# Kernel tuning notes

Measured on AMD Instinct MI355X. Metric: run time of the kernel, lower is better.

Reference implementation:

```python
import jax, jax.numpy as jnp
import numpy as np
import math

N_EMBD = 1024
N_HEAD = 16
HEAD_SIZE = N_EMBD // N_HEAD
LAYER_IDX = 2
LAMBDA_INIT = 0.8 - 0.6 * math.exp(-0.3 * (LAYER_IDX - 1))
LN_EPS = 1e-5
B, T = 4, 1024


def setup_inputs() -> dict:
    key = jax.random.key(0)
    ks = jax.random.split(key, 11)
    s = 0.02  # weight init scale
    return {
        "x": jax.random.normal(ks[0], (B, T, N_EMBD), dtype=jnp.float32),
        "Wq1": jax.random.normal(ks[1], (N_EMBD, N_EMBD), dtype=jnp.float32) * s,
        "Wq2": jax.random.normal(ks[2], (N_EMBD, N_EMBD), dtype=jnp.float32) * s,
        "Wk1": jax.random.normal(ks[3], (N_EMBD, N_EMBD), dtype=jnp.float32) * s,
        "Wk2": jax.random.normal(ks[4], (N_EMBD, N_EMBD), dtype=jnp.float32) * s,
        "Wv": jax.random.normal(ks[5], (N_EMBD, 2 * N_EMBD), dtype=jnp.float32) * s,
        "Wc": jax.random.normal(ks[6], (2 * N_EMBD, N_EMBD), dtype=jnp.float32) * s,
        "lq1": jax.random.normal(ks[7], (N_HEAD, HEAD_SIZE), dtype=jnp.float32) * 0.1,
        "lk1": jax.random.normal(ks[8], (N_HEAD, HEAD_SIZE), dtype=jnp.float32) * 0.1,
        "lq2": jax.random.normal(ks[9], (N_HEAD, HEAD_SIZE), dtype=jnp.float32) * 0.1,
        "lk2": jax.random.normal(ks[10], (N_HEAD, HEAD_SIZE), dtype=jnp.float32) * 0.1,
    }


def reference(x, Wq1, Wq2, Wk1, Wk2, Wv, Wc, lq1, lk1, lq2, lk2):
    Bx, Tx, C = x.shape
    H, hs = N_HEAD, HEAD_SIZE
    scale = 1.0 / math.sqrt(hs)

    # projections -> (B, T, H, d)
    q1 = (x @ Wq1).reshape(Bx, Tx, H, hs)
    q2 = (x @ Wq2).reshape(Bx, Tx, H, hs)
    k1 = (x @ Wk1).reshape(Bx, Tx, H, hs)
    k2 = (x @ Wk2).reshape(Bx, Tx, H, hs)
    v = (x @ Wv).reshape(Bx, Tx, H, 2 * hs)

    # dual score streams (B, H, T, T)
    att1 = jnp.einsum("bqhd,bkhd->bhqk", q1, k1) * scale
    att2 = jnp.einsum("bqhd,bkhd->bhqk", q2, k2) * scale

    causal = jnp.tril(jnp.ones((Tx, Tx), dtype=bool))  # (T, T)
    neg_inf = jnp.float32(-jnp.inf)
    att1 = jnp.where(causal, att1, neg_inf)
    att2 = jnp.where(causal, att2, neg_inf)
    a1 = jax.nn.softmax(att1, axis=-1)
    a2 = jax.nn.softmax(att2, axis=-1)

    # per-head differential lambda
    lam1 = jnp.exp(jnp.sum(lq1 * lk1, axis=-1))  # (H,)
    lam2 = jnp.exp(jnp.sum(lq2 * lk2, axis=-1))  # (H,)
    lam_full = lam1 - lam2 + LAMBDA_INIT  # (H,)

    att = a1 - lam_full[None, :, None, None] * a2  # dropout = identity (eval)

    # PV matmul -> (B, T, H, 2*hs)
    y = jnp.einsum("bhqk,bkhd->bqhd", att, v)

    # subLN over last dim (no affine)
    mu = jnp.mean(y, axis=-1, keepdims=True)
    var = jnp.mean(jnp.square(y - mu), axis=-1, keepdims=True)
    y = (y - mu) / jnp.sqrt(var + LN_EPS)
    y = y * (1.0 - LAMBDA_INIT)

    y = y.reshape(Bx, Tx, 2 * C)
    return y @ Wc  # resid dropout = identity (eval)
```

## Files before the change

kernel.cpp:

```cpp
#include <hip/hip_runtime.h>


#define T_SEQ 1024
#define NH 16
#define DV 128
#define NPROJ 6144
#define KSTR 72

typedef __bf16 bf16_t;
typedef __bf16 bf16x8 __attribute__((ext_vector_type(8)));
typedef __bf16 bf16x4 __attribute__((ext_vector_type(4)));
typedef __bf16 bf16x2 __attribute__((ext_vector_type(2)));
typedef _Float16 f16x4 __attribute__((ext_vector_type(4)));
typedef _Float16 f16x2 __attribute__((ext_vector_type(2)));
typedef short s16x4 __attribute__((ext_vector_type(4)));
typedef float f32x4 __attribute__((ext_vector_type(4)));

#define LAMBDA_INIT 0.35550906759096928f
#define ONE_MINUS_LI 0.6444909324090307f
#define LOG2E 1.4426950408889634f
#define RTHR 44.36f

#if __has_builtin(__builtin_amdgcn_mfma_f32_16x16x16_bf16)
#define MFMA16(a, b, c) __builtin_amdgcn_mfma_f32_16x16x16_bf16(a, b, c, 0, 0, 0)
#elif __has_builtin(__builtin_amdgcn_mfma_f32_16x16x16bf16_1k)
#define MFMA16(a, b, c)                                                       \
  __builtin_amdgcn_mfma_f32_16x16x16bf16_1k(                                  \
      __builtin_bit_cast(s16x4, a), __builtin_bit_cast(s16x4, b), c, 0, 0, 0)
#else
#define MFMA16(a, b, c) (c)
#endif

#define MFMA32(a, b, c) __builtin_amdgcn_mfma_f32_16x16x32_bf16(a, b, c, 0, 0, 0)

#define GLDS(g, l)                                                            \
  __builtin_amdgcn_global_load_lds(                                           \
      (const __attribute__((address_space(1))) void*)(g),                     \
      (__attribute__((address_space(3))) void*)(l), 16, 0, 0)

static const size_t OFF_WCAT = 0;
static const size_t OFF_XB = OFF_WCAT + (size_t)6144 * 1024 * 2;
static const size_t OFF_WCT = OFF_XB + (size_t)4096 * 1024 * 2;
static const size_t OFF_PROJ = OFF_WCT + (size_t)2048 * 1024 * 2;
static const size_t OFF_VT = OFF_PROJ + (size_t)4096 * 6144 * 2;
static const size_t OFF_YLN = OFF_VT + (size_t)64 * 128 * 1024 * 2;
static const size_t OFF_LAM = OFF_YLN + (size_t)4096 * 2048 * 2;

__global__ void __launch_bounds__(256) cast_x(const float* __restrict__ x,
                                              bf16_t* __restrict__ o) {
  const int i = (blockIdx.x * 256 + threadIdx.x) * 4;
  float4 v = *(const float4*)(x + i);
  bf16x4 r = {(bf16_t)v.x, (bf16_t)v.y, (bf16_t)v.z, (bf16_t)v.w};
  *(bf16x4*)(o + i) = r;
}

__device__ __forceinline__ void tcast_body(const float* __restrict__ W,
                                           bf16_t* __restrict__ Wt, int K,
                                           int N, int row0) {
  __shared__ float tile[32][33];
  const int k0 = blockIdx.x * 32, n0 = blockIdx.y * 32;
  const int tx = threadIdx.x & 31, ty = threadIdx.x >> 5;
#pragma unroll
  for (int i = 0; i < 32; i += 8)
    tile[ty + i][tx] = W[(long)(k0 + ty + i) * N + n0 + tx];
  __syncthreads();
#pragma unroll
  for (int i = 0; i < 32; i += 8)
    Wt[(long)(row0 + n0 + ty + i) * K + k0 + tx] = (bf16_t)tile[tx][ty + i];
}

__global__ void __launch_bounds__(256) tcast_w(const float* __restrict__ W,
                                               bf16_t* __restrict__ Wt, int K,
                                               int N, int row0) {
  tcast_body(W, Wt, K, N, row0);
}

__global__ void __launch_bounds__(256) tcast_w4(const float* __restrict__ W0,
                                                const float* __restrict__ W1,
                                                const float* __restrict__ W2,
                                                const float* __restrict__ W3,
                                                bf16_t* __restrict__ Wt) {
  const float* Ws[4] = {W0, W1, W2, W3};
  tcast_body(Ws[blockIdx.z], Wt, 1024, 1024, blockIdx.z * 1024);
}

__global__ void lam_kernel(const float* __restrict__ lq1,
                           const float* __restrict__ lk1,
                           const float* __restrict__ lq2,
                           const float* __restrict__ lk2,
                           float* __restrict__ lam) {
  const int h = threadIdx.x;
  if (h < NH) {
    float d1 = 0.f, d2 = 0.f;
    for (int i = 0; i < 64; ++i) {
      d1 += lq1[h * 64 + i] * lk1[h * 64 + i];
      d2 += lq2[h * 64 + i] * lk2[h * 64 + i];
    }
    lam[h] = expf(d1) - expf(d2) + LAMBDA_INIT;
  }
}

#define GBM 256
#define GBN 256
#define GBK 64

__global__ void __launch_bounds__(512, 1) gemm256(const bf16_t* __restrict__ A,
                                                  const bf16_t* __restrict__ Bt,
                                                  bf16_t* __restrict__ C,
                                                  int M, int N, int K,
                                                  int nbx) {
  __shared__ __align__(16) bf16_t As[2][GBM * GBK];
  __shared__ __align__(16) bf16_t Bs[2][GBN * GBK];
  const int tid = threadIdx.x;
  const int w = tid >> 6, lane = tid & 63;
  const int quad = lane >> 4, l16 = lane & 15;
  const int wr = w >> 2, wc = w & 3;

  const int wg = blockIdx.x;
  const int cpx = gridDim.x >> 3;
  const int sw = (wg & 7) * cpx + (wg >> 3);
  const int by = sw / nbx, bx = sw % nbx;
  const int m0 = by * GBM, n0 = bx * GBN;

  const int r8 = lane >> 3, g = lane & 7;
  const int gsw = (g ^ r8) * 8;
  const bf16_t* gA[4];
  const bf16_t* gB[4];
#pragma unroll
  for (int j = 0; j < 4; ++j) {
    gA[j] = A + (long)(m0 + w * 32 + j * 8 + r8) * K + gsw;
    gB[j] = Bt + (long)(n0 + w * 32 + j * 8 + r8) * K + gsw;
  }

  const int kx = (l16 & 7) << 4;
  const int ko0 = (quad * 16) ^ kx;
  const int ko1 = (64 + quad * 16) ^ kx;

  f32x4 acc[8][4] = {};

  const int nt = K >> 6;

#pragma unroll
  for (int j = 0; j < 4; ++j) {
    GLDS(gA[j], As[0] + (w * 32 + j * 8) * GBK);
    GLDS(gB[j], Bs[0] + (w * 32 + j * 8) * GBK);
  }
  asm volatile("s_waitcnt vmcnt(0)" ::: "memory");
  __builtin_amdgcn_s_barrier();

  for (int t = 0; t < nt; ++t) {
    const bf16_t* Ab = (t & 1) ? As[1] : As[0];
    const bf16_t* Bb = (t & 1) ? Bs[1] : Bs[0];
    bf16_t* Asb = (t & 1) ? As[0] : As[1];
    bf16_t* Bsb = (t & 1) ? Bs[0] : Bs[1];
    const bool pf = (t + 1 < nt);
    const long ko = (long)(t + 1) * GBK;

    const char* Arow = (const char*)Ab + (size_t)(wr * 128 + l16) * 128;
    const char* Brow = (const char*)Bb + (size_t)(wc * 64 + l16) * 128;

    bf16x8 af[4][2], bn0[2][2], bn1[2][2];

#pragma unroll
    for (int mt = 0; mt < 4; ++mt) {
      af[mt][0] = *(const bf16x8*)(Arow + (size_t)mt * 16 * 128 + ko0);
      af[mt][1] = *(const bf16x8*)(Arow + (size_t)mt * 16 * 128 + ko1);
    }
#pragma unroll
    for (int n = 0; n < 2; ++n) {
      bn0[n][0] = *(const bf16x8*)(Brow + (size_t)n * 16 * 128 + ko0);
      bn0[n][1] = *(const bf16x8*)(Brow + (size_t)n * 16 * 128 + ko1);
    }
    if (pf) {
      GLDS(gA[0] + ko, Asb + (w * 32) * GBK);
      GLDS(gB[0] + ko, Bsb + (w * 32) * GBK);
      GLDS(gA[1] + ko, Asb + (w * 32 + 8) * GBK);
      GLDS(gB[1] + ko, Bsb + (w * 32 + 8) * GBK);
    }
    __builtin_amdgcn_s_barrier();
    __builtin_amdgcn_s_setprio(1);
#pragma unroll
    for (int mt = 0; mt < 4; ++mt)
#pragma unroll
      for (int n = 0; n < 2; ++n) {
        acc[mt][n] = MFMA32(af[mt][0], bn0[n][0], acc[mt][n]);
        acc[mt][n] = MFMA32(af[mt][1], bn0[n][1], acc[mt][n]);
      }
    __builtin_amdgcn_s_setprio(0);
    __builtin_amdgcn_s_barrier();

#pragma unroll
    for (int n = 0; n < 2; ++n) {
      bn1[n][0] = *(const bf16x8*)(Brow + (size_t)(32 + n * 16) * 128 + ko0);
      bn1[n][1] = *(const bf16x8*)(Brow + (size_t)(32 + n * 16) * 128 + ko1);
    }
    if (pf) {
      GLDS(gA[2] + ko, Asb + (w * 32 + 16) * GBK);
      GLDS(gB[2] + ko, Bsb + (w * 32 + 16) * GBK);
      GLDS(gA[3] + ko, Asb + (w * 32 + 24) * GBK);
      GLDS(gB[3] + ko, Bsb + (w * 32 + 24) * GBK);
    }
    __builtin_amdgcn_s_barrier();
    __builtin_amdgcn_s_setprio(1);
#pragma unroll
    for (int mt = 0; mt < 4; ++mt)
#pragma unroll
      for (int n = 0; n < 2; ++n) {
        acc[mt][2 + n] = MFMA32(af[mt][0], bn1[n][0], acc[mt][2 + n]);
        acc[mt][2 + n] = MFMA32(af[mt][1], bn1[n][1], acc[mt][2 + n]);
      }
    __builtin_amdgcn_s_setprio(0);
    __builtin_amdgcn_s_barrier();

#pragma unroll
    for (int mt = 0; mt < 4; ++mt) {
      af[mt][0] = *(const bf16x8*)(Arow + (size_t)(64 + mt * 16) * 128 + ko0);
      af[mt][1] = *(const bf16x8*)(Arow + (size_t)(64 + mt * 16) * 128 + ko1);
    }
    __builtin_amdgcn_s_barrier();
    __builtin_amdgcn_s_setprio(1);
#pragma unroll
    for (int mt = 0; mt < 4; ++mt)
#pragma unroll
      for (int n = 0; n < 2; ++n) {
        acc[4 + mt][2 + n] = MFMA32(af[mt][0], bn1[n][0], acc[4 + mt][2 + n]);
        acc[4 + mt][2 + n] = MFMA32(af[mt][1], bn1[n][1], acc[4 + mt][2 + n]);
      }
    __builtin_amdgcn_s_setprio(0);
    __builtin_amdgcn_s_barrier();

    __builtin_amdgcn_s_setprio(1);
#pragma unroll
    for (int mt = 0; mt < 4; ++mt)
#pragma unroll
      for (int n = 0; n < 2; ++n) {
        acc[4 + mt][n] = MFMA32(af[mt][0], bn0[n][0], acc[4 + mt][n]);
        acc[4 + mt][n] = MFMA32(af[mt][1], bn0[n][1], acc[4 + mt][n]);
      }
    __builtin_amdgcn_s_setprio(0);

    asm volatile("s_waitcnt vmcnt(0)" ::: "memory");
    __builtin_amdgcn_s_barrier();
  }

#pragma unroll
  for (int mt = 0; mt < 8; ++mt)
#pragma unroll
    for (int n = 0; n < 4; ++n) {
      const int col = n0 + wc * 64 + n * 16 + l16;
#pragma unroll
      for (int i = 0; i < 4; ++i) {
        const int row = m0 + wr * 128 + mt * 16 + quad * 4 + i;
        C[(long)row * N + col] = (bf16_t)acc[mt][n][i];
      }
    }
}

#define BM 128
#define BK 32

template <typename OutT>
__global__ void __launch_bounds__(256) gemm_bt_n64(const bf16_t* __restrict__ A,
                                                   const bf16_t* __restrict__ Bt,
                                                   OutT* __restrict__ C, int M,
                                                   int N, int K) {
  __shared__ __align__(16) bf16_t As[BM * BK];
  __shared__ __align__(16) bf16_t Bs[64 * BK];
  const int tid = threadIdx.x;
  const int w = tid >> 6;
  const int lane = tid & 63;
  const int quad = lane >> 4, l16 = lane & 15;
  const int m0 = blockIdx.y * BM, n0 = blockIdx.x * 64;
  const int wm = (w >> 1) * 64, wn = (w & 1) * 32;
  const int srow = tid >> 2;
  const int scol = (tid & 3) * 8;

  const bf16_t* Ag0 = A + (long)(m0 + srow) * K + scol;
  const bf16_t* Ag1 = Ag0 + (long)64 * K;
  const bf16_t* Bg0 = Bt + (long)(n0 + srow) * K + scol;
  bf16_t* lA0 = As + tid * 8;
  bf16_t* lA1 = As + 2048 + tid * 8;
  bf16_t* lB0 = Bs + tid * 8;

  f32x4 acc[4][2] = {};

  for (int k0 = 0; k0 < K; k0 += BK) {
    GLDS(Ag0 + k0, lA0);
    GLDS(Ag1 + k0, lA1);
    GLDS(Bg0 + k0, lB0);
    __syncthreads();
    bf16x8 af[4], bfr[2];
#pragma unroll
    for (int t = 0; t < 4; ++t)
      af[t] = *(const bf16x8*)(As + (wm + t * 16 + l16) * BK + quad * 8);
#pragma unroll
    for (int t = 0; t < 2; ++t)
      bfr[t] = *(const bf16x8*)(Bs + (wn + t * 16 + l16) * BK + quad * 8);
#pragma unroll
    for (int mt = 0; mt < 4; ++mt)
#pragma unroll
      for (int ntt = 0; ntt < 2; ++ntt)
        acc[mt][ntt] = MFMA32(af[mt], bfr[ntt], acc[mt][ntt]);
    __syncthreads();
  }

#pragma unroll
  for (int mt = 0; mt < 4; ++mt)
#pragma unroll
    for (int ntt = 0; ntt < 2; ++ntt) {
      const int col = n0 + wn + ntt * 16 + l16;
#pragma unroll
      for (int i = 0; i < 4; ++i) {
        const int row = m0 + wm + mt * 16 + quad * 4 + i;
        C[(long)row * N + col] = (OutT)acc[mt][ntt][i];
      }
    }
}

__global__ void __launch_bounds__(256) transpose_v(const bf16_t* __restrict__ proj,
                                                   bf16_t* __restrict__ vt) {
  __shared__ bf16_t tile[32][34];
  const int bh = blockIdx.z;
  const int b = bh >> 4, h = bh & 15;
  const int t0 = blockIdx.x * 32, d0 = blockIdx.y * 32;
  const int tx = threadIdx.x & 31, ty = threadIdx.x >> 5;
  const bf16_t* src = proj + (long)(b * T_SEQ) * NPROJ + 4096 + h * 128;
#pragma unroll
  for (int i = 0; i < 32; i += 8)
    tile[ty + i][tx] = src[(long)(t0 + ty + i) * NPROJ + d0 + tx];
  __syncthreads();
  bf16_t* dst = vt + ((long)bh * DV) * T_SEQ;
#pragma unroll
  for (int i = 0; i < 32; i += 8)
    dst[(long)(d0 + ty + i) * T_SEQ + t0 + tx] = tile[tx][ty + i];
}

__global__ void __launch_bounds__(256) attn_kernel(const bf16_t* __restrict__ proj,
                                                   const bf16_t* __restrict__ vt,
                                                   _Float16* __restrict__ a1,
                                                   _Float16* __restrict__ a2) {
  const int x = blockIdx.x;
  const int qblk = 15 - (x >> 7);
  const int st = (x >> 6) & 1;
  const int bh = x & 63;
  const int b = bh >> 4, h = bh & 15;
  const int tid = threadIdx.x;
  const int w = tid >> 6, lane = tid & 63;
  const int quad = lane >> 4, l16 = lane & 15;
  const long bT = (long)b * T_SEQ;

  __shared__ __align__(16) bf16_t Ks[64 * KSTR];
  __shared__ __align__(16) bf16_t Vs[DV * KSTR];

  const int koff = h * 64 + 2048 + st * 1024;
  const bf16_t* gK = proj + (bT + (tid >> 2)) * (long)NPROJ + koff + (tid & 3) * 16;
  const bf16_t* gV = vt + (long)bh * DV * T_SEQ + (long)(tid >> 1) * T_SEQ +
                     (tid & 1) * 32;
  const int kwK = (tid >> 2) * KSTR + (tid & 3) * 16;
  const int kwV = (tid >> 1) * KSTR + (tid & 1) * 32;

  const float sc = 0.125f * LOG2E;
  const int q0 = qblk * 64 + w * 16;
  const int qg = q0 + l16;

  const bf16_t* qrow = proj + (bT + qg) * (long)NPROJ + h * 64 + st * 1024;
  bf16x8 aq[2];
  aq[0] = *(const bf16x8*)(qrow + quad * 8);
  aq[1] = *(const bf16x8*)(qrow + 32 + quad * 8);

  f32x4 O[8] = {};
  float m = -3.0e38f, l = 0.f;
  const bf16x4 one4 = {(bf16_t)1.0f, (bf16_t)1.0f, (bf16_t)1.0f, (bf16_t)1.0f};

  const int kend_blk = qblk * 64 + 64;
  const int kend_w = q0 + 16;

  bf16x8 rK[2], rV[4];
  rK[0] = *(const bf16x8*)(gK);
  rK[1] = *(const bf16x8*)(gK + 8);
#pragma unroll
  for (int j = 0; j < 4; ++j) rV[j] = *(const bf16x8*)(gV + j * 8);

  for (int kt = 0; kt < kend_blk; kt += 64) {
    *(bf16x8*)(Ks + kwK) = rK[0];
    *(bf16x8*)(Ks + kwK + 8) = rK[1];
#pragma unroll
    for (int j = 0; j < 4; ++j) *(bf16x8*)(Vs + kwV + j * 8) = rV[j];
    __syncthreads();

    if (kt + 64 < kend_blk) {
      const long ko = (long)(kt + 64) * NPROJ;
      rK[0] = *(const bf16x8*)(gK + ko);
      rK[1] = *(const bf16x8*)(gK + ko + 8);
#pragma unroll
      for (int j = 0; j < 4; ++j)
        rV[j] = *(const bf16x8*)(gV + kt + 64 + j * 8);
    }

    if (kt < kend_w) {
      f32x4 s[4];
#pragma unroll
      for (int c = 0; c < 4; ++c) {
        const bf16_t* kr = Ks + (c * 16 + l16) * KSTR;
        bf16x8 ka0 = *(const bf16x8*)(kr + quad * 8);
        bf16x8 ka1 = *(const bf16x8*)(kr + 32 + quad * 8);
        f32x4 z = {};
        z = MFMA32(ka0, aq[0], z);
        z = MFMA32(ka1, aq[1], z);
        s[c] = z;
      }
      if (kt + 63 > q0) {
#pragma unroll
        for (int c = 0; c < 4; ++c)
#pragma unroll
          for (int i = 0; i < 4; ++i) {
            const int key = kt + c * 16 + quad * 4 + i;
            if (key > qg) s[c][i] = -1e30f;
          }
      }
      float t[4];
#pragma unroll
      for (int c = 0; c < 4; ++c)
        t[c] = fmaxf(fmaxf(s[c][0], s[c][1]), fmaxf(s[c][2], s[c][3]));
      float mx = fmaxf(fmaxf(t[0], t[1]), fmaxf(t[2], t[3]));
      mx = fmaxf(mx, __shfl_xor(mx, 16));
      mx = fmaxf(mx, __shfl_xor(mx, 32));
      if (!__all(mx <= m + RTHR)) {
        const float mn = fmaxf(m, mx);
        const float al = exp2f((m - mn) * sc);
        m = mn;
#pragma unroll
        for (int f = 0; f < 8; ++f)
#pragma unroll
          for (int i = 0; i < 4; ++i) O[f][i] *= al;
        l *= al;
      }
      const float ms = m * sc;
      bf16x4 pc[4];
#pragma unroll
      for (int c = 0; c < 4; ++c)
#pragma unroll
        for (int i = 0; i < 4; ++i)
          pc[c][i] = (bf16_t)exp2f(fmaf(s[c][i], sc, -ms));
      f32x4 la = {};
#pragma unroll
      for (int c = 0; c < 4; ++c) la = MFMA16(one4, pc[c], la);
#pragma unroll
      for (int c = 0; c < 4; ++c) {
#pragma unroll
        for (int f = 0; f < 8; ++f) {
          bf16x4 va =
              *(const bf16x4*)(Vs + (f * 16 + l16) * KSTR + c * 16 + quad * 4);
          O[f] = MFMA16(va, pc[c], O[f]);
        }
      }
      l += la[0];
    }
    __syncthreads();
  }

  const float inv = 1.0f / l;
  _Float16* ob = st ? a2 : a1;
  _Float16* dst = ob + ((bT + qg) * 16 + h) * (long)128 + quad * 4;
#pragma unroll
  for (int f = 0; f < 8; ++f) {
    f16x4 o = {(_Float16)(O[f][0] * inv), (_Float16)(O[f][1] * inv),
               (_Float16)(O[f][2] * inv), (_Float16)(O[f][3] * inv)};
    *(f16x4*)(dst + f * 16) = o;
  }
}

__global__ void __launch_bounds__(256) combine_kernel(const _Float16* __restrict__ a1,
                                                      const _Float16* __restrict__ a2,
                                                      const float* __restrict__ lamp,
                                                      bf16_t* __restrict__ yln) {
  const int unit = blockIdx.x * 4 + (threadIdx.x >> 6);
  const int lane = threadIdx.x & 63;
  const float lam = lamp[unit & 15];
  const long base = (long)unit * 128 + lane * 2;
  f16x2 v1 = *(const f16x2*)(a1 + base);
  f16x2 v2 = *(const f16x2*)(a2 + base);
  float y0 = (float)v1[0] - lam * (float)v2[0];
  float y1 = (float)v1[1] - lam * (float)v2[1];
  float sm = y0 + y1, sq = y0 * y0 + y1 * y1;
#pragma unroll
  for (int off = 1; off < 64; off <<= 1) {
    sm += __shfl_xor(sm, off);
    sq += __shfl_xor(sq, off);
  }
  const float mu = sm * (1.0f / 128.0f);
  const float var = sq * (1.0f / 128.0f) - mu * mu;
  const float rs = rsqrtf(var + 1e-5f) * ONE_MINUS_LI;
  bf16x2 o = {(bf16_t)((y0 - mu) * rs), (bf16_t)((y1 - mu) * rs)};
  *(bf16x2*)(yln + base) = o;
}

extern "C" void kernel_launch(void* const* d_in, const int* in_sizes, int n_in,
                              void* d_out, int out_size, void* d_ws,
                              size_t ws_size, hipStream_t stream) {
  const float* x = (const float*)d_in[0];
  const float* Wq1 = (const float*)d_in[1];
  const float* Wq2 = (const float*)d_in[2];
  const float* Wk1 = (const float*)d_in[3];
  const float* Wk2 = (const float*)d_in[4];
  const float* Wv = (const float*)d_in[5];
  const float* Wc = (const float*)d_in[6];
  const float* lq1 = (const float*)d_in[7];
  const float* lk1 = (const float*)d_in[8];
  const float* lq2 = (const float*)d_in[9];
  const float* lk2 = (const float*)d_in[10];
  float* out = (float*)d_out;

  char* ws = (char*)d_ws;
  bf16_t* wcat = (bf16_t*)(ws + OFF_WCAT);
  bf16_t* xb = (bf16_t*)(ws + OFF_XB);
  bf16_t* wct = (bf16_t*)(ws + OFF_WCT);
  bf16_t* projb = (bf16_t*)(ws + OFF_PROJ);
  bf16_t* vtb = (bf16_t*)(ws + OFF_VT);
  bf16_t* ylnb = (bf16_t*)(ws + OFF_YLN);
  float* lamp = (float*)(ws + OFF_LAM);
  _Float16* a1b = (_Float16*)(ws + OFF_YLN);
  _Float16* a2b = (_Float16*)(ws + OFF_WCAT);

  cast_x<<<4096, 256, 0, stream>>>(x, xb);
  tcast_w4<<<dim3(32, 32, 4), 256, 0, stream>>>(Wq1, Wq2, Wk1, Wk2, wcat);
  tcast_w<<<dim3(32, 64), 256, 0, stream>>>(Wv, wcat, 1024, 2048, 4096);
  tcast_w<<<dim3(64, 32), 256, 0, stream>>>(Wc, wct, 2048, 1024, 0);
  lam_kernel<<<1, 64, 0, stream>>>(lq1, lk1, lq2, lk2, lamp);

  gemm256<<<dim3(384), 512, 0, stream>>>(xb, wcat, projb, 4096, 6144, 1024, 24);
  transpose_v<<<dim3(32, 4, 64), 256, 0, stream>>>(projb, vtb);
  attn_kernel<<<dim3(2048), 256, 0, stream>>>(projb, vtb, a1b, a2b);
  combine_kernel<<<dim3(16384), 256, 0, stream>>>(a1b, a2b, lamp, ylnb);
  gemm_bt_n64<float><<<dim3(16, 32), 256, 0, stream>>>(ylnb, wct, out, 4096, 1024, 2048);
}
```

Measured before the change: 304.5 us.

## Pair causal q-blocks per attention block, permute V layout, widen output GEMM tile

Each attention workgroup now processes two complementary query blocks (15-p and p) sequentially, so the causal triangle's work is balanced per block and half as many blocks are launched. The V transpose writes keys in a permuted order so the PV loop can fetch 8 bf16 per LDS read and split them across two 16x16x16 MFMAs. The final projection GEMM uses 128x128 tiles instead of 128x64, raising per-wave reuse. In exchange there are fewer blocks for latency hiding and more accumulator registers in the GEMM.

```diff
diff --git a/kernel.cpp b/kernel.cpp
--- a/kernel.cpp
+++ b/kernel.cpp
@@ -257,62 +257,65 @@
 }
 
 #define BM 128
+#define BN 128
 #define BK 32
 
 template <typename OutT>
-__global__ void __launch_bounds__(256) gemm_bt_n64(const bf16_t* __restrict__ A,
-                                                   const bf16_t* __restrict__ Bt,
-                                                   OutT* __restrict__ C, int M,
-                                                   int N, int K) {
+__global__ void __launch_bounds__(256) gemm_bt(const bf16_t* __restrict__ A,
+                                               const bf16_t* __restrict__ Bt,
+                                               OutT* __restrict__ C, int M,
+                                               int N, int K) {
   __shared__ __align__(16) bf16_t As[BM * BK];
-  __shared__ __align__(16) bf16_t Bs[64 * BK];
+  __shared__ __align__(16) bf16_t Bs[BN * BK];
   const int tid = threadIdx.x;
   const int w = tid >> 6;
   const int lane = tid & 63;
   const int quad = lane >> 4, l16 = lane & 15;
-  const int m0 = blockIdx.y * BM, n0 = blockIdx.x * 64;
-  const int wm = (w >> 1) * 64, wn = (w & 1) * 32;
+  const int m0 = blockIdx.y * BM, n0 = blockIdx.x * BN;
+  const int wm = (w >> 1) * 64, wn = (w & 1) * 64;
   const int srow = tid >> 2;
   const int scol = (tid & 3) * 8;
 
   const bf16_t* Ag0 = A + (long)(m0 + srow) * K + scol;
   const bf16_t* Ag1 = Ag0 + (long)64 * K;
   const bf16_t* Bg0 = Bt + (long)(n0 + srow) * K + scol;
+  const bf16_t* Bg1 = Bg0 + (long)64 * K;
   bf16_t* lA0 = As + tid * 8;
   bf16_t* lA1 = As + 2048 + tid * 8;
   bf16_t* lB0 = Bs + tid * 8;
-
-  f32x4 acc[4][2] = {};
+  bf16_t* lB1 = Bs + 2048 + tid * 8;
+
+  f32x4 acc[4][4] = {};
 
   for (int k0 = 0; k0 < K; k0 += BK) {
     GLDS(Ag0 + k0, lA0);
     GLDS(Ag1 + k0, lA1);
     GLDS(Bg0 + k0, lB0);
+    GLDS(Bg1 + k0, lB1);
     __syncthreads();
-    bf16x8 af[4], bfr[2];
-#pragma unroll
-    for (int t = 0; t < 4; ++t)
+    bf16x8 af[4], bfr[4];
+#pragma unroll
+    for (int t = 0; t < 4; ++t) {
       af[t] = *(const bf16x8*)(As + (wm + t * 16 + l16) * BK + quad * 8);
-#pragma unroll
-    for (int t = 0; t < 2; ++t)
       bfr[t] = *(const bf16x8*)(Bs + (wn + t * 16 + l16) * BK + quad * 8);
+    }
 #pragma unroll
     for (int mt = 0; mt < 4; ++mt)
 #pragma unroll
-      for (int ntt = 0; ntt < 2; ++ntt)
-        acc[mt][ntt] = MFMA32(af[mt], bfr[ntt], acc[mt][ntt]);
+      for (int nt = 0; nt < 4; ++nt)
+        acc[mt][nt] = MFMA32(af[mt], bfr[nt], acc[mt][nt]);
     __syncthreads();
   }
 
 #pragma unroll
   for (int mt = 0; mt < 4; ++mt)
 #pragma unroll
-    for (int ntt = 0; ntt < 2; ++ntt) {
-      const int col = n0 + wn + ntt * 16 + l16;
+    for (int nt = 0; nt < 4; ++nt) {
+      const int col = n0 + wn + nt * 16 + l16;
 #pragma unroll
       for (int i = 0; i < 4; ++i) {
         const int row = m0 + wm + mt * 16 + quad * 4 + i;
-        C[(long)row * N + col] = (OutT)acc[mt][ntt][i];
+        C[(long)row * N + col] = (OutT)acc[mt][nt][i];
       }
     }
 }
@@ -329,10 +332,14 @@
   for (int i = 0; i < 32; i += 8)
     tile[ty + i][tx] = src[(long)(t0 + ty + i) * NPROJ + d0 + tx];
   __syncthreads();
-  bf16_t* dst = vt + ((long)bh * DV) * T_SEQ;
-#pragma unroll
-  for (int i = 0; i < 32; i += 8)
-    dst[(long)(d0 + ty + i) * T_SEQ + t0 + tx] = tile[tx][ty + i];
+  const int d_loc = threadIdx.x >> 3;
+  const int g = threadIdx.x & 7;
+  const int s = g >> 2, qd = g & 3;
+  const int tl = s * 16 + qd * 4;
+  bf16x4 o = {tile[tl + 0][d_loc], tile[tl + 1][d_loc], tile[tl + 2][d_loc],
+              tile[tl + 3][d_loc]};
+  bf16_t* dst = vt + (long)bh * (DV * T_SEQ) + (long)(d0 + d_loc) * T_SEQ;
+  *(bf16x4*)(dst + t0 + qd * 8 + s * 4) = o;
 }
 
 __global__ void __launch_bounds__(256) attn_kernel(const bf16_t* __restrict__ proj,
@@ -340,7 +347,7 @@
                                                    _Float16* __restrict__ a1,
                                                    _Float16* __restrict__ a2) {
   const int x = blockIdx.x;
-  const int qblk = 15 - (x >> 7);
+  const int p = x >> 7;
   const int st = (x >> 6) & 1;
   const int bh = x & 63;
   const int b = bh >> 4, h = bh & 15;
@@ -354,119 +361,128 @@
 
   const int koff = h * 64 + 2048 + st * 1024;
   const bf16_t* gK = proj + (bT + (tid >> 2)) * (long)NPROJ + koff + (tid & 3) * 16;
-  const bf16_t* gV = vt + (long)bh * DV * T_SEQ + (long)(tid >> 1) * T_SEQ +
-                     (tid & 1) * 32;
+  const bf16_t* gV = vt + (long)bh * DV * T_SEQ + (long)(tid >> 3) * T_SEQ +
+                     (tid & 7) * 8;
   const int kwK = (tid >> 2) * KSTR + (tid & 3) * 16;
-  const int kwV = (tid >> 1) * KSTR + (tid & 1) * 32;
+  const int kwV = (tid >> 3) * KSTR + (tid & 7) * 8;
 
   const float sc = 0.125f * LOG2E;
-  const int q0 = qblk * 64 + w * 16;
-  const int qg = q0 + l16;
-
-  const bf16_t* qrow = proj + (bT + qg) * (long)NPROJ + h * 64 + st * 1024;
-  bf16x8 aq[2];
-  aq[0] = *(const bf16x8*)(qrow + quad * 8);
-  aq[1] = *(const bf16x8*)(qrow + 32 + quad * 8);
-
-  f32x4 O[8] = {};
-  float m = -3.0e38f, l = 0.f;
   const bf16x4 one4 = {(bf16_t)1.0f, (bf16_t)1.0f, (bf16_t)1.0f, (bf16_t)1.0f};
 
-  const int kend_blk = qblk * 64 + 64;
-  const int kend_w = q0 + 16;
-
-  bf16x8 rK[2], rV[4];
-  rK[0] = *(const bf16x8*)(gK);
-  rK[1] = *(const bf16x8*)(gK + 8);
-#pragma unroll
-  for (int j = 0; j < 4; ++j) rV[j] = *(const bf16x8*)(gV + j * 8);
-
-  for (int kt = 0; kt < kend_blk; kt += 64) {
-    *(bf16x8*)(Ks + kwK) = rK[0];
-    *(bf16x8*)(Ks + kwK + 8) = rK[1];
-#pragma unroll
-    for (int j = 0; j < 4; ++j) *(bf16x8*)(Vs + kwV + j * 8) = rV[j];
-    __syncthreads();
-
-    if (kt + 64 < kend_blk) {
-      const long ko = (long)(kt + 64) * NPROJ;
-      rK[0] = *(const bf16x8*)(gK + ko);
-      rK[1] = *(const bf16x8*)(gK + ko + 8);
+  for (int ph = 0; ph < 2; ++ph) {
+    const int qblk = ph ? p : 15 - p;
+    const int q0 = qblk * 64 + w * 16;
+    const int qg = q0 + l16;
+
+    const bf16_t* qrow = proj + (bT + qg) * (long)NPROJ + h * 64 + st * 1024;
+    bf16x8 aq[2];
+    aq[0] = *(const bf16x8*)(qrow + quad * 8);
+    aq[1] = *(const bf16x8*)(qrow + 32 + quad * 8);
+
+    f32x4 O[8] = {};
+    float m = -3.0e38f, l = 0.f;
+
+    const int kend_blk = qblk * 64 + 64;
+    const int kend_w = q0 + 16;
+
+    bf16x8 rK[2], rV[4];
+    rK[0] = *(const bf16x8*)(gK);
+    rK[1] = *(const bf16x8*)(gK + 8);
+#pragma unroll
+    for (int j = 0; j < 4; ++j)
+      rV[j] = *(const bf16x8*)(gV + (long)(32 * j) * T_SEQ);
+
+    for (int kt = 0; kt < kend_blk; kt += 64) {
+      *(bf16x8*)(Ks + kwK) = rK[0];
+      *(bf16x8*)(Ks + kwK + 8) = rK[1];
 #pragma unroll
       for (int j = 0; j < 4; ++j)
-        rV[j] = *(const bf16x8*)(gV + kt + 64 + j * 8);
-    }
-
-    if (kt < kend_w) {
-      f32x4 s[4];
-#pragma unroll
-      for (int c = 0; c < 4; ++c) {
-        const bf16_t* kr = Ks + (c * 16 + l16) * KSTR;
-        bf16x8 ka0 = *(const bf16x8*)(kr + quad * 8);
-        bf16x8 ka1 = *(const bf16x8*)(kr + 32 + quad * 8);
-        f32x4 z = {};
-        z = MFMA32(ka0, aq[0], z);
-        z = MFMA32(ka1, aq[1], z);
-        s[c] = z;
-      }
-      if (kt + 63 > q0) {
+        *(bf16x8*)(Vs + kwV + j * 32 * KSTR) = rV[j];
+      __syncthreads();
+
+      if (kt + 64 < kend_blk) {
+        const long ko = (long)(kt + 64) * NPROJ;
+        rK[0] = *(const bf16x8*)(gK + ko);
+        rK[1] = *(const bf16x8*)(gK + ko + 8);
+#pragma unroll
+        for (int j = 0; j < 4; ++j)
+          rV[j] = *(const bf16x8*)(gV + kt + 64 + (long)(32 * j) * T_SEQ);
+      }
+
+      if (kt < kend_w) {
+        f32x4 s[4];
+#pragma unroll
+        for (int c = 0; c < 4; ++c) {
+          const bf16_t* kr = Ks + (c * 16 + l16) * KSTR;
+          bf16x8 ka0 = *(const bf16x8*)(kr + quad * 8);
+          bf16x8 ka1 = *(const bf16x8*)(kr + 32 + quad * 8);
+          f32x4 z = {};
+          z = MFMA32(ka0, aq[0], z);
+          z = MFMA32(ka1, aq[1], z);
+          s[c] = z;
+        }
+        if (kt + 63 > q0) {
+#pragma unroll
+          for (int c = 0; c < 4; ++c)
+#pragma unroll
+            for (int i = 0; i < 4; ++i) {
+              const int key = kt + c * 16 + quad * 4 + i;
+              if (key > qg) s[c][i] = -1e30f;
+            }
+        }
+        float t[4];
 #pragma unroll
         for (int c = 0; c < 4; ++c)
-#pragma unroll
-          for (int i = 0; i < 4; ++i) {
-            const int key = kt + c * 16 + quad * 4 + i;
-            if (key > qg) s[c][i] = -1e30f;
+          t[c] = fmaxf(fmaxf(s[c][0], s[c][1]), fmaxf(s[c][2], s[c][3]));
+        float mx = fmaxf(fmaxf(t[0], t[1]), fmaxf(t[2], t[3]));
+        mx = fmaxf(mx, __shfl_xor(mx, 16));
+        mx = fmaxf(mx, __shfl_xor(mx, 32));
+        if (!__all(mx <= m + RTHR)) {
+          const float mn = fmaxf(m, mx);
+          const float al = exp2f((m - mn) * sc);
+          m = mn;
+#pragma unroll
+          for (int f = 0; f < 8; ++f)
+#pragma unroll
+            for (int i = 0; i < 4; ++i) O[f][i] *= al;
+          l *= al;
+        }
+        const float ms = m * sc;
+        bf16x4 pc[4];
+#pragma unroll
+        for (int c = 0; c < 4; ++c)
+#pragma unroll
+          for (int i = 0; i < 4; ++i)
+            pc[c][i] = (bf16_t)exp2f(fmaf(s[c][i], sc, -ms));
+        f32x4 la = {};
+#pragma unroll
+        for (int c = 0; c < 4; ++c) la = MFMA16(one4, pc[c], la);
+#pragma unroll
+        for (int cp = 0; cp < 2; ++cp) {
+#pragma unroll
+          for (int f = 0; f < 8; ++f) {
+            bf16x8 va = *(const bf16x8*)(Vs + (f * 16 + l16) * KSTR +
+                                         cp * 32 + quad * 8);
+            bf16x4 lo = __builtin_shufflevector(va, va, 0, 1, 2, 3);
+            bf16x4 hi = __builtin_shufflevector(va, va, 4, 5, 6, 7);
+            O[f] = MFMA16(lo, pc[2 * cp], O[f]);
+            O[f] = MFMA16(hi, pc[2 * cp + 1], O[f]);
           }
-      }
-      float t[4];
-#pragma unroll
-      for (int c = 0; c < 4; ++c)
-        t[c] = fmaxf(fmaxf(s[c][0], s[c][1]), fmaxf(s[c][2], s[c][3]));
-      float mx = fmaxf(fmaxf(t[0], t[1]), fmaxf(t[2], t[3]));
-      mx = fmaxf(mx, __shfl_xor(mx, 16));
-      mx = fmaxf(mx, __shfl_xor(mx, 32));
-      if (!__all(mx <= m + RTHR)) {
-        const float mn = fmaxf(m, mx);
-        const float al = exp2f((m - mn) * sc);
-        m = mn;
-#pragma unroll
-        for (int f = 0; f < 8; ++f)
-#pragma unroll
-          for (int i = 0; i < 4; ++i) O[f][i] *= al;
-        l *= al;
-      }
-      const float ms = m * sc;
-      bf16x4 pc[4];
-#pragma unroll
-      for (int c = 0; c < 4; ++c)
-#pragma unroll
-        for (int i = 0; i < 4; ++i)
-          pc[c][i] = (bf16_t)exp2f(fmaf(s[c][i], sc, -ms));
-      f32x4 la = {};
-#pragma unroll
-      for (int c = 0; c < 4; ++c) la = MFMA16(one4, pc[c], la);
-#pragma unroll
-      for (int c = 0; c < 4; ++c) {
-#pragma unroll
-        for (int f = 0; f < 8; ++f) {
-          bf16x4 va =
-              *(const bf16x4*)(Vs + (f * 16 + l16) * KSTR + c * 16 + quad * 4);
-          O[f] = MFMA16(va, pc[c], O[f]);
         }
-      }
-      l += la[0];
-    }
-    __syncthreads();
-  }
-
-  const float inv = 1.0f / l;
-  _Float16* ob = st ? a2 : a1;
-  _Float16* dst = ob + ((bT + qg) * 16 + h) * (long)128 + quad * 4;
-#pragma unroll
-  for (int f = 0; f < 8; ++f) {
-    f16x4 o = {(_Float16)(O[f][0] * inv), (_Float16)(O[f][1] * inv),
-               (_Float16)(O[f][2] * inv), (_Float16)(O[f][3] * inv)};
-    *(f16x4*)(dst + f * 16) = o;
+        l += la[0];
+      }
+      __syncthreads();
+    }
+
+    const float inv = 1.0f / l;
+    _Float16* ob = st ? a2 : a1;
+    _Float16* dst = ob + ((bT + qg) * 16 + h) * (long)128 + quad * 4;
+#pragma unroll
+    for (int f = 0; f < 8; ++f) {
+      f16x4 o = {(_Float16)(O[f][0] * inv), (_Float16)(O[f][1] * inv),
+                 (_Float16)(O[f][2] * inv), (_Float16)(O[f][3] * inv)};
+      *(f16x4*)(dst + f * 16) = o;
+    }
   }
 }
 
@@ -530,7 +546,7 @@
 
   gemm256<<<dim3(384), 512, 0, stream>>>(xb, wcat, projb, 4096, 6144, 1024, 24);
   transpose_v<<<dim3(32, 4, 64), 256, 0, stream>>>(projb, vtb);
-  attn_kernel<<<dim3(2048), 256, 0, stream>>>(projb, vtb, a1b, a2b);
+  attn_kernel<<<dim3(1024), 256, 0, stream>>>(projb, vtb, a1b, a2b);
   combine_kernel<<<dim3(16384), 256, 0, stream>>>(a1b, a2b, lamp, ylnb);
-  gemm_bt_n64<float><<<dim3(16, 32), 256, 0, stream>>>(ylnb, wct, out, 4096, 1024, 2048);
-}
+  gemm_bt<float><<<dim3(8, 32), 256, 0, stream>>>(ylnb, wct, out, 4096, 1024, 2048);
+}
```

Measured after the change: 316.7 us. +4.0%, slower.

## Merge prep kernels, fold lambda into combine, widen output GEMM tile

Applied to the files above, without the earlier changes.

Merges the x cast and all the weight transpose-casts into one prep kernel, and computes the per-head lambda inside combine_kernel with wave shuffles. This removes five launches and the separate lam kernel. The output GEMM tile grows from 128x64 to 128x128, which halves the grid to 256 blocks and doubles reuse of the A tile. In exchange, combine repeats the lambda reduction in every wave, and the larger GEMM tile uses more registers while running fewer blocks on the device.

```diff
diff --git a/kernel.cpp b/kernel.cpp
--- a/kernel.cpp
+++ b/kernel.cpp
@@ -44,21 +44,56 @@
 static const size_t OFF_PROJ = OFF_WCT + (size_t)2048 * 1024 * 2;
 static const size_t OFF_VT = OFF_PROJ + (size_t)4096 * 6144 * 2;
 static const size_t OFF_YLN = OFF_VT + (size_t)64 * 128 * 1024 * 2;
-static const size_t OFF_LAM = OFF_YLN + (size_t)4096 * 2048 * 2;
-
-__global__ void __launch_bounds__(256) cast_x(const float* __restrict__ x,
-                                              bf16_t* __restrict__ o) {
-  const int i = (blockIdx.x * 256 + threadIdx.x) * 4;
-  float4 v = *(const float4*)(x + i);
-  bf16x4 r = {(bf16_t)v.x, (bf16_t)v.y, (bf16_t)v.z, (bf16_t)v.w};
-  *(bf16x4*)(o + i) = r;
-}
-
-__device__ __forceinline__ void tcast_body(const float* __restrict__ W,
-                                           bf16_t* __restrict__ Wt, int K,
-                                           int N, int row0) {
+
+__global__ void __launch_bounds__(256) prep_kernel(
+    const float* __restrict__ x, const float* __restrict__ Wq1,
+    const float* __restrict__ Wq2, const float* __restrict__ Wk1,
+    const float* __restrict__ Wk2, const float* __restrict__ Wv,
+    const float* __restrict__ Wc, bf16_t* __restrict__ xb,
+    bf16_t* __restrict__ wcat, bf16_t* __restrict__ wct) {
   __shared__ float tile[32][33];
-  const int k0 = blockIdx.x * 32, n0 = blockIdx.y * 32;
+  const int b = blockIdx.x;
+  if (b < 4096) {
+    const int i = (b * 256 + threadIdx.x) * 4;
+    float4 v = *(const float4*)(x + i);
+    bf16x4 r = {(bf16_t)v.x, (bf16_t)v.y, (bf16_t)v.z, (bf16_t)v.w};
+    *(bf16x4*)(xb + i) = r;
+    return;
+  }
+  const float* W;
+  bf16_t* Wt;
+  int K, N, row0, k0, n0;
+  if (b < 8192) {
+    int idx = b - 4096;
+    const int z = idx >> 10;
+    idx &= 1023;
+    const float* Ws[4] = {Wq1, Wq2, Wk1, Wk2};
+    W = Ws[z];
+    Wt = wcat;
+    K = 1024;
+    N = 1024;
+    row0 = z * 1024;
+    k0 = (idx & 31) * 32;
+    n0 = (idx >> 5) * 32;
+  } else if (b < 10240) {
+    const int idx = b - 8192;
+    W = Wv;
+    Wt = wcat;
+    K = 1024;
+    N = 2048;
+    row0 = 4096;
+    k0 = (idx & 31) * 32;
+    n0 = (idx >> 5) * 32;
+  } else {
+    const int idx = b - 10240;
+    W = Wc;
+    Wt = wct;
+    K = 2048;
+    N = 1024;
+    row0 = 0;
+    k0 = (idx & 63) * 32;
+    n0 = (idx >> 6) * 32;
+  }
   const int tx = threadIdx.x & 31, ty = threadIdx.x >> 5;
 #pragma unroll
   for (int i = 0; i < 32; i += 8)
@@ -67,37 +102,6 @@
 #pragma unroll
   for (int i = 0; i < 32; i += 8)
     Wt[(long)(row0 + n0 + ty + i) * K + k0 + tx] = (bf16_t)tile[tx][ty + i];
-}
-
-__global__ void __launch_bounds__(256) tcast_w(const float* __restrict__ W,
-                                               bf16_t* __restrict__ Wt, int K,
-                                               int N, int row0) {
-  tcast_body(W, Wt, K, N, row0);
-}
-
-__global__ void __launch_bounds__(256) tcast_w4(const float* __restrict__ W0,
-                                                const float* __restrict__ W1,
-                                                const float* __restrict__ W2,
-                                                const float* __restrict__ W3,
-                                                bf16_t* __restrict__ Wt) {
-  const float* Ws[4] = {W0, W1, W2, W3};
-  tcast_body(Ws[blockIdx.z], Wt, 1024, 1024, blockIdx.z * 1024);
-}
-
-__global__ void lam_kernel(const float* __restrict__ lq1,
-                           const float* __restrict__ lk1,
-                           const float* __restrict__ lq2,
-                           const float* __restrict__ lk2,
-                           float* __restrict__ lam) {
-  const int h = threadIdx.x;
-  if (h < NH) {
-    float d1 = 0.f, d2 = 0.f;
-    for (int i = 0; i < 64; ++i) {
-      d1 += lq1[h * 64 + i] * lk1[h * 64 + i];
-      d2 += lq2[h * 64 + i] * lk2[h * 64 + i];
-    }
-    lam[h] = expf(d1) - expf(d2) + LAMBDA_INIT;
-  }
 }
 
 #define GBM 256
@@ -257,62 +261,65 @@
 }
 
 #define BM 128
+#define BN 128
 #define BK 32
 
 template <typename OutT>
-__global__ void __launch_bounds__(256) gemm_bt_n64(const bf16_t* __restrict__ A,
-                                                   const bf16_t* __restrict__ Bt,
-                                                   OutT* __restrict__ C, int M,
-                                                   int N, int K) {
+__global__ void __launch_bounds__(256) gemm_bt(const bf16_t* __restrict__ A,
+                                               const bf16_t* __restrict__ Bt,
+                                               OutT* __restrict__ C, int M,
+                                               int N, int K) {
   __shared__ __align__(16) bf16_t As[BM * BK];
-  __shared__ __align__(16) bf16_t Bs[64 * BK];
+  __shared__ __align__(16) bf16_t Bs[BN * BK];
   const int tid = threadIdx.x;
   const int w = tid >> 6;
   const int lane = tid & 63;
   const int quad = lane >> 4, l16 = lane & 15;
-  const int m0 = blockIdx.y * BM, n0 = blockIdx.x * 64;
-  const int wm = (w >> 1) * 64, wn = (w & 1) * 32;
+  const int m0 = blockIdx.y * BM, n0 = blockIdx.x * BN;
+  const int wm = (w >> 1) * 64, wn = (w & 1) * 64;
   const int srow = tid >> 2;
   const int scol = (tid & 3) * 8;
 
   const bf16_t* Ag0 = A + (long)(m0 + srow) * K + scol;
   const bf16_t* Ag1 = Ag0 + (long)64 * K;
   const bf16_t* Bg0 = Bt + (long)(n0 + srow) * K + scol;
+  const bf16_t* Bg1 = Bg0 + (long)64 * K;
   bf16_t* lA0 = As + tid * 8;
   bf16_t* lA1 = As + 2048 + tid * 8;
   bf16_t* lB0 = Bs + tid * 8;
-
-  f32x4 acc[4][2] = {};
+  bf16_t* lB1 = Bs + 2048 + tid * 8;
+
+  f32x4 acc[4][4] = {};
 
   for (int k0 = 0; k0 < K; k0 += BK) {
     GLDS(Ag0 + k0, lA0);
     GLDS(Ag1 + k0, lA1);
     GLDS(Bg0 + k0, lB0);
+    GLDS(Bg1 + k0, lB1);
     __syncthreads();
-    bf16x8 af[4], bfr[2];
-#pragma unroll
-    for (int t = 0; t < 4; ++t)
+    bf16x8 af[4], bfr[4];
+#pragma unroll
+    for (int t = 0; t < 4; ++t) {
       af[t] = *(const bf16x8*)(As + (wm + t * 16 + l16) * BK + quad * 8);
-#pragma unroll
-    for (int t = 0; t < 2; ++t)
       bfr[t] = *(const bf16x8*)(Bs + (wn + t * 16 + l16) * BK + quad * 8);
+    }
 #pragma unroll
     for (int mt = 0; mt < 4; ++mt)
 #pragma unroll
-      for (int ntt = 0; ntt < 2; ++ntt)
-        acc[mt][ntt] = MFMA32(af[mt], bfr[ntt], acc[mt][ntt]);
+      for (int nt = 0; nt < 4; ++nt)
+        acc[mt][nt] = MFMA32(af[mt], bfr[nt], acc[mt][nt]);
     __syncthreads();
   }
 
 #pragma unroll
   for (int mt = 0; mt < 4; ++mt)
 #pragma unroll
-    for (int ntt = 0; ntt < 2; ++ntt) {
-      const int col = n0 + wn + ntt * 16 + l16;
+    for (int nt = 0; nt < 4; ++nt) {
+      const int col = n0 + wn + nt * 16 + l16;
 #pragma unroll
       for (int i = 0; i < 4; ++i) {
         const int row = m0 + wm + mt * 16 + quad * 4 + i;
-        C[(long)row * N + col] = (OutT)acc[mt][ntt][i];
+        C[(long)row * N + col] = (OutT)acc[mt][nt][i];
       }
     }
 }
@@ -470,13 +477,23 @@
   }
 }
 
-__global__ void __launch_bounds__(256) combine_kernel(const _Float16* __restrict__ a1,
-                                                      const _Float16* __restrict__ a2,
-                                                      const float* __restrict__ lamp,
-                                                      bf16_t* __restrict__ yln) {
+__global__ void __launch_bounds__(256) combine_kernel(
+    const _Float16* __restrict__ a1, const _Float16* __restrict__ a2,
+    const float* __restrict__ lq1, const float* __restrict__ lk1,
+    const float* __restrict__ lq2, const float* __restrict__ lk2,
+    bf16_t* __restrict__ yln) {
   const int unit = blockIdx.x * 4 + (threadIdx.x >> 6);
   const int lane = threadIdx.x & 63;
-  const float lam = lamp[unit & 15];
+  const int h = unit & 15;
+  float p1 = lq1[h * 64 + lane] * lk1[h * 64 + lane];
+  float p2 = lq2[h * 64 + lane] * lk2[h * 64 + lane];
+#pragma unroll
+  for (int off = 1; off < 64; off <<= 1) {
+    p1 += __shfl_xor(p1, off);
+    p2 += __shfl_xor(p2, off);
+  }
+  const float lam = expf(p1) - expf(p2) + LAMBDA_INIT;
+
   const long base = (long)unit * 128 + lane * 2;
   f16x2 v1 = *(const f16x2*)(a1 + base);
   f16x2 v2 = *(const f16x2*)(a2 + base);
@@ -518,19 +535,15 @@
   bf16_t* projb = (bf16_t*)(ws + OFF_PROJ);
   bf16_t* vtb = (bf16_t*)(ws + OFF_VT);
   bf16_t* ylnb = (bf16_t*)(ws + OFF_YLN);
-  float* lamp = (float*)(ws + OFF_LAM);
   _Float16* a1b = (_Float16*)(ws + OFF_YLN);
   _Float16* a2b = (_Float16*)(ws + OFF_WCAT);
 
-  cast_x<<<4096, 256, 0, stream>>>(x, xb);
-  tcast_w4<<<dim3(32, 32, 4), 256, 0, stream>>>(Wq1, Wq2, Wk1, Wk2, wcat);
-  tcast_w<<<dim3(32, 64), 256, 0, stream>>>(Wv, wcat, 1024, 2048, 4096);
-  tcast_w<<<dim3(64, 32), 256, 0, stream>>>(Wc, wct, 2048, 1024, 0);
-  lam_kernel<<<1, 64, 0, stream>>>(lq1, lk1, lq2, lk2, lamp);
-
+  prep_kernel<<<dim3(12288), 256, 0, stream>>>(x, Wq1, Wq2, Wk1, Wk2, Wv, Wc,
+                                               xb, wcat, wct);
   gemm256<<<dim3(384), 512, 0, stream>>>(xb, wcat, projb, 4096, 6144, 1024, 24);
   transpose_v<<<dim3(32, 4, 64), 256, 0, stream>>>(projb, vtb);
   attn_kernel<<<dim3(2048), 256, 0, stream>>>(projb, vtb, a1b, a2b);
-  combine_kernel<<<dim3(16384), 256, 0, stream>>>(a1b, a2b, lamp, ylnb);
-  gemm_bt_n64<float><<<dim3(16, 32), 256, 0, stream>>>(ylnb, wct, out, 4096, 1024, 2048);
-}
+  combine_kernel<<<dim3(16384), 256, 0, stream>>>(a1b, a2b, lq1, lk1, lq2, lk2,
+                                                  ylnb);
+  gemm_bt<float><<<dim3(8, 32), 256, 0, stream>>>(ylnb, wct, out, 4096, 1024, 2048);
+}
```

Measured after the change: 317.6 us. 1.04x slower.
